# Kernel optimization log

Hardware: AMD Instinct MI355X
Metric: run time of the kernel (lower is better)

Reference implementation:

```python
import jax, jax.numpy as jnp
import numpy as np
import math

B, S, D, H, L, F, V, C = 8, 1024, 768, 12, 6, 3072, 32000, 10
DK = D // H
EPS = 1e-5


def _pos_encoding(seq_len, d):
    pos = jnp.arange(seq_len, dtype=jnp.float32)[:, None]
    div = jnp.exp(jnp.arange(0, d, 2, dtype=jnp.float32) * (-math.log(10000.0) / d))
    pe = jnp.zeros((seq_len, d), dtype=jnp.float32)
    pe = pe.at[:, 0::2].set(jnp.sin(pos * div))
    pe = pe.at[:, 1::2].set(jnp.cos(pos * div))
    return pe


def _layernorm(x, scale, bias):
    mu = jnp.mean(x, axis=-1, keepdims=True)
    var = jnp.mean(jnp.square(x - mu), axis=-1, keepdims=True)
    return (x - mu) * jax.lax.rsqrt(var + EPS) * scale + bias


def setup_inputs() -> dict:
    key = jax.random.key(0)
    ks = jax.random.split(key, 14)
    s = 0.02
    return {
        "tokens": jax.random.randint(ks[0], (B, S), 0, V),
        "emb": jax.random.normal(ks[1], (V, D), jnp.float32) * s,
        "Wq": jax.random.normal(ks[2], (L, D, D), jnp.float32) * s,
        "Wk": jax.random.normal(ks[3], (L, D, D), jnp.float32) * s,
        "Wv": jax.random.normal(ks[4], (L, D, D), jnp.float32) * s,
        "Wo": jax.random.normal(ks[5], (L, D, D), jnp.float32) * s,
        "W1": jax.random.normal(ks[6], (L, D, F), jnp.float32) * s,
        "W2": jax.random.normal(ks[7], (L, F, D), jnp.float32) * s,
        "ln1_s": jnp.ones((L, D), jnp.float32),
        "ln1_b": jnp.zeros((L, D), jnp.float32),
        "ln2_s": jnp.ones((L, D), jnp.float32),
        "ln2_b": jnp.zeros((L, D), jnp.float32),
        "Wc": jax.random.normal(ks[8], (D, C), jnp.float32) * s,
        "bc": jnp.zeros((C,), jnp.float32),
    }


def _block(x, p):
    Wq, Wk, Wv, Wo, W1, W2, l1s, l1b, l2s, l2b = p
    b, s = x.shape[0], x.shape[1]
    q = (x @ Wq).reshape(b, s, H, DK)
    k = (x @ Wk).reshape(b, s, H, DK)
    v = (x @ Wv).reshape(b, s, H, DK)
    scores = jnp.einsum("bqhd,bkhd->bhqk", q, k) / math.sqrt(DK)
    attn = jax.nn.softmax(scores, axis=-1)
    out = jnp.einsum("bhqk,bkhd->bqhd", attn, v).reshape(b, s, D) @ Wo
    x = _layernorm(x + out, l1s, l1b)
    ffn = jax.nn.relu(x @ W1) @ W2
    x = _layernorm(x + ffn, l2s, l2b)
    return x


def reference(tokens, emb, Wq, Wk, Wv, Wo, W1, W2, ln1_s, ln1_b, ln2_s, ln2_b, Wc, bc):
    x = emb[tokens] + _pos_encoding(tokens.shape[1], D)[None]

    def step(h, p):
        return _block(h, p), None

    x, _ = jax.lax.scan(step, x, (Wq, Wk, Wv, Wo, W1, W2, ln1_s, ln1_b, ln2_s, ln2_b))
    pooled = jnp.mean(x, axis=1)  # [B, D]
    return pooled @ Wc + bc
```

## Files before the change

### kernel.cpp

```cpp
#include <hip/hip_runtime.h>
#include <hip/hip_bf16.h>
#include <math.h>

#define BB 8
#define SS 1024
#define DD 768
#define HH 12
#define LL 6
#define FF 3072
#define CC 10
#define BS_ (BB * SS)

typedef __attribute__((ext_vector_type(8))) short short8v;
typedef __attribute__((ext_vector_type(4))) float f32x4;
typedef __attribute__((ext_vector_type(16))) float f32x16;
typedef __attribute__((ext_vector_type(8))) unsigned short ushort8v;
typedef __attribute__((ext_vector_type(4))) unsigned short ushort4v;
typedef __attribute__((ext_vector_type(4))) unsigned int uint4v;

__device__ inline unsigned short f2bf(float f) {
  unsigned int u = __builtin_bit_cast(unsigned int, f);
  u += 0x7fffu + ((u >> 16) & 1u);
  return (unsigned short)(u >> 16);
}
__device__ inline float bf2f(unsigned short u) {
  return __builtin_bit_cast(float, (unsigned int)u << 16);
}
__device__ inline unsigned int cvtpk(float lo, float hi) {
  unsigned int r;
  asm("v_cvt_pk_bf16_f32 %0, %1, %2" : "=v"(r) : "v"(lo), "v"(hi));
  return r;
}
__device__ inline void plswap(unsigned int& a, unsigned int& b) {
  asm volatile("v_permlane32_swap_b32 %0, %1" : "+v"(a), "+v"(b));
}
__device__ inline void gload16(const void* g, void* l) {
  __builtin_amdgcn_global_load_lds((const __attribute__((address_space(1))) void*)g,
                                   (__attribute__((address_space(3))) void*)l, 16, 0, 0);
}

__device__ inline float wave_sum(float v) {
#pragma unroll
  for (int off = 32; off > 0; off >>= 1) v += __shfl_down(v, off);
  return v;
}

__global__ __launch_bounds__(256) void k_embed(const int* __restrict__ tokens,
                                               const float* __restrict__ emb,
                                               ushort* __restrict__ xb) {
  int row = blockIdx.x;
  int s = row & (SS - 1);
  int tok = tokens[row];
  const float* e = emb + (size_t)tok * DD;
  ushort* xbr = xb + (size_t)row * DD;
  for (int d = threadIdx.x; d < DD; d += 256) {
    float freq = expf((float)(d & ~1) * -0.0119926306f);
    float ang = (float)s * freq;
    float pe = (d & 1) ? cosf(ang) : sinf(ang);
    xbr[d] = f2bf(e[d] + pe);
  }
}

__global__ __launch_bounds__(256) void k_transpose_all(
    const float* __restrict__ wq, const float* __restrict__ wk,
    const float* __restrict__ wv, const float* __restrict__ wo,
    const float* __restrict__ w1, const float* __restrict__ w2,
    ushort* __restrict__ wqkv_t, ushort* __restrict__ wo_t,
    ushort* __restrict__ w1_t, ushort* __restrict__ w2_t) {
  __shared__ float tile[32][33];
  int bid = blockIdx.x;
  const float* W; ushort* Wt; int K, N, lb;
  if (bid < 1728) {
    int m = bid / 576; lb = bid - m * 576;
    W = (m == 0) ? wq : (m == 1) ? wk : wv;
    Wt = wqkv_t + m * 768 * 768; K = 768; N = 768;
  } else if (bid < 2304) {
    W = wo; Wt = wo_t; K = 768; N = 768; lb = bid - 1728;
  } else if (bid < 4608) {
    W = w1; Wt = w1_t; K = 768; N = 3072; lb = bid - 2304;
  } else {
    W = w2; Wt = w2_t; K = 3072; N = 768; lb = bid - 4608;
  }
  int nbk = K >> 5;
  int k0 = (lb % nbk) * 32, n0 = (lb / nbk) * 32;
  int t = threadIdx.x;
  int r = t >> 3, c4 = (t & 7) * 4;
  float4 v = *(const float4*)(W + (size_t)(k0 + r) * N + n0 + c4);
  tile[r][c4 + 0] = v.x; tile[r][c4 + 1] = v.y;
  tile[r][c4 + 2] = v.z; tile[r][c4 + 3] = v.w;
  __syncthreads();
  ushort4v o;
#pragma unroll
  for (int i = 0; i < 4; ++i) o[i] = f2bf(tile[c4 + i][r]);
  *(ushort4v*)(Wt + (size_t)(n0 + r) * K + k0 + c4) = o;
}

template <int RELU, int TN>
__global__ __launch_bounds__(256) void k_gemm_db(const ushort* __restrict__ A,
                                                 const ushort* __restrict__ Bt,
                                                 ushort* __restrict__ Cout,
                                                 int M, int N, int K) {
  constexpr int NF = TN / 32;
  __shared__ ushort smem[2][(128 + TN) * 64];
  int bidl = blockIdx.y * gridDim.x + blockIdx.x;
  int nwg = gridDim.x * gridDim.y;
  int cpx = nwg >> 3;
  int tid = (bidl & 7) * cpx + (bidl >> 3);
  int n0 = (tid % gridDim.x) * TN, m0 = (tid / gridDim.x) * 128;
  int t = threadIdx.x, w = t >> 6, l = t & 63;
  int wr = (w >> 1) * 64, wc = (w & 1) * (TN / 2);
  int lr = l & 15, lg = l >> 4;
  f32x4 acc[4][NF] = {};
  int sr8 = l >> 3;
  int scw = ((l & 7) ^ sr8) * 8;
  const ushort* ag = A + (size_t)(m0 + w * 8 + sr8) * K + scw;
  const ushort* bg = Bt + (size_t)(n0 + w * 8 + sr8) * K + scw;
  int nk = K >> 6;
  {
    ushort* al = &smem[0][(w * 8) * 64];
    ushort* bl = &smem[0][128 * 64 + (w * 8) * 64];
#pragma unroll
    for (int ii = 0; ii < 4; ++ii) gload16(ag + (size_t)ii * 32 * K, al + ii * 2048);
#pragma unroll
    for (int ii = 0; ii < TN / 32; ++ii) gload16(bg + (size_t)ii * 32 * K, bl + ii * 2048);
  }
  int rsw = lr & 7;
  for (int k = 0; k < nk; ++k) {
    __syncthreads();
    if (k + 1 < nk) {
      int kb = (k + 1) & 1;
      int kc0 = (k + 1) * 64;
      ushort* al = &smem[kb][(w * 8) * 64];
      ushort* bl = &smem[kb][128 * 64 + (w * 8) * 64];
#pragma unroll
      for (int ii = 0; ii < 4; ++ii) gload16(ag + (size_t)ii * 32 * K + kc0, al + ii * 2048);
#pragma unroll
      for (int ii = 0; ii < TN / 32; ++ii) gload16(bg + (size_t)ii * 32 * K + kc0, bl + ii * 2048);
    }
    const ushort* As = &smem[k & 1][0];
    const ushort* Bs = &smem[k & 1][128 * 64];
#pragma unroll
    for (int ks = 0; ks < 2; ++ks) {
      short8v af[4], bfr[NF];
#pragma unroll
      for (int mi = 0; mi < 4; ++mi)
        af[mi] = *(const short8v*)(As + (wr + mi * 16 + lr) * 64 + (((ks * 4 + lg) ^ rsw) << 3));
#pragma unroll
      for (int ni = 0; ni < NF; ++ni)
        bfr[ni] = *(const short8v*)(Bs + (wc + ni * 16 + lr) * 64 + (((ks * 4 + lg) ^ rsw) << 3));
      __builtin_amdgcn_s_setprio(1);
#pragma unroll
      for (int mi = 0; mi < 4; ++mi)
#pragma unroll
        for (int ni = 0; ni < NF; ++ni)
          acc[mi][ni] = __builtin_amdgcn_mfma_f32_16x16x32_bf16(af[mi], bfr[ni], acc[mi][ni], 0, 0, 0);
      __builtin_amdgcn_s_setprio(0);
    }
  }
  __syncthreads();
  ushort* cst = &smem[0][0];
#pragma unroll
  for (int mi = 0; mi < 4; ++mi)
#pragma unroll
    for (int ni = 0; ni < NF; ++ni) {
      int cl = wc + ni * 16 + lr;
#pragma unroll
      for (int i = 0; i < 4; ++i) {
        int rl = wr + mi * 16 + lg * 4 + i;
        float v = acc[mi][ni][i];
        if (RELU) v = fmaxf(v, 0.f);
        cst[rl * TN + (cl ^ (((rl >> 2) & 3) << 4))] = f2bf(v);
      }
    }
  __syncthreads();
  {
    int row = t >> 1, half = t & 1;
    int swr = ((row >> 2) & 3) << 4;
    ushort* crow = Cout + (size_t)(m0 + row) * N + n0 + half * (TN / 2);
#pragma unroll
    for (int c8 = 0; c8 < TN / 16; ++c8) {
      int c = half * (TN / 2) + c8 * 8;
      ushort8v vv = *(const ushort8v*)(&cst[row * TN + (c ^ swr)]);
      *(ushort8v*)(crow + c8 * 8) = vv;
    }
  }
}

__global__ __launch_bounds__(256) void k_flash(const ushort* __restrict__ qkv,
                                               ushort* __restrict__ ao) {
  __shared__ ushort Ks[2][64][64];
  __shared__ ushort Vt[2][64][64];
  const int LD = 2304;
  int bidl = blockIdx.y * gridDim.x + blockIdx.x;
  int tid = (bidl & 7) * 96 + (bidl >> 3);
  int qt = tid & 7;
  int bh = tid >> 3;
  int hd = bh % HH, b = bh / HH;
  int t = threadIdx.x, w = t >> 6, l = t & 63;
  int q = l & 31, hl = l >> 5;
  int q0 = qt * 128;
  const ushort* qbase = qkv + (size_t)(b * SS) * LD + hd * 64;
  const ushort* kbase = qbase + 768;
  const ushort* vbase = qbase + 1536;
  short8v qfb[4];
  {
    const ushort* qrow = qbase + (size_t)(q0 + w * 32 + q) * LD + hl * 8;
    qfb[0] = *(const short8v*)(qrow);
    qfb[1] = *(const short8v*)(qrow + 16);
    qfb[2] = *(const short8v*)(qrow + 32);
    qfb[3] = *(const short8v*)(qrow + 48);
  }
  const float CEXP = 0.125f * 1.44269504f;
  float l_run = 0.f;
  f32x16 o_acc[2] = {};
  int r8_ = l >> 3;
  const ushort* kgA = kbase + (size_t)(w * 16 + r8_) * LD +
                      (((l & 7) ^ r8_ ^ ((2 * w) & 3)) * 8);
  const ushort* kgB = kbase + (size_t)(w * 16 + 8 + r8_) * LD +
                      (((l & 7) ^ r8_ ^ ((2 * w + 1) & 3)) * 8);
  int d_ = t & 7;
  int dk0 = d_ * 8;
  int kv2 = (t >> 3) * 2;
  const ushort* vg = vbase + (size_t)kv2 * LD + dk0;
  {
    gload16(kgA, &Ks[0][w * 16][0]);
    gload16(kgB, &Ks[0][w * 16 + 8][0]);
    ushort8v v0 = *(const ushort8v*)(vg);
    ushort8v v1 = *(const ushort8v*)(vg + LD);
#pragma unroll
    for (int i = 0; i < 8; ++i) {
      unsigned int pk = (unsigned int)v0[i] | ((unsigned int)v1[i] << 16);
      *(unsigned int*)(&Vt[0][dk0 + i][kv2 ^ (((i ^ d_) & 7) << 3)]) = pk;
    }
  }
  for (int kt = 0; kt < 16; ++kt) {
    int cur = kt & 1, nxt = cur ^ 1;
    __syncthreads();
    ushort8v v0n, v1n;
    if (kt < 15) {
      size_t off = (size_t)(kt + 1) * 64 * LD;
      gload16(kgA + off, &Ks[nxt][w * 16][0]);
      gload16(kgB + off, &Ks[nxt][w * 16 + 8][0]);
      const ushort* vgn = vg + off;
      v0n = *(const ushort8v*)(vgn);
      v1n = *(const ushort8v*)(vgn + LD);
    }
    f32x16 s[2] = {};
    __builtin_amdgcn_s_setprio(1);
#pragma unroll
    for (int c = 0; c < 4; ++c)
#pragma unroll
      for (int mi = 0; mi < 2; ++mi) {
        int gr = ((c << 1) | hl) ^ (l & 7) ^ ((l >> 3) & 3);
        short8v kf = *(const short8v*)(&Ks[cur][mi * 32 + q][gr << 3]);
        s[mi] = __builtin_amdgcn_mfma_f32_32x32x16_bf16(kf, qfb[c], s[mi], 0, 0, 0);
      }
    __builtin_amdgcn_s_setprio(0);
    float psum = 0.f;
#pragma unroll
    for (int mi = 0; mi < 2; ++mi)
#pragma unroll
      for (int r = 0; r < 16; ++r) {
        float e = exp2f(s[mi][r] * CEXP);
        s[mi][r] = e;
        psum += e;
      }
    psum += __shfl_xor(psum, 32);
    l_run += psum;
    short8v pfb[4];
#pragma unroll
    for (int mi = 0; mi < 2; ++mi)
#pragma unroll
      for (int k2 = 0; k2 < 2; ++k2) {
        unsigned int a0 = cvtpk(s[mi][8 * k2 + 0], s[mi][8 * k2 + 1]);
        unsigned int a1 = cvtpk(s[mi][8 * k2 + 2], s[mi][8 * k2 + 3]);
        unsigned int b0 = cvtpk(s[mi][8 * k2 + 4], s[mi][8 * k2 + 5]);
        unsigned int b1 = cvtpk(s[mi][8 * k2 + 6], s[mi][8 * k2 + 7]);
        plswap(a0, b0);
        plswap(a1, b1);
        uint4v u;
        u[0] = a0; u[1] = a1; u[2] = b0; u[3] = b1;
        pfb[mi * 2 + k2] = __builtin_bit_cast(short8v, u);
      }
    if (kt < 15) {
#pragma unroll
      for (int i = 0; i < 8; ++i) {
        unsigned int pk = (unsigned int)v0n[i] | ((unsigned int)v1n[i] << 16);
        *(unsigned int*)(&Vt[nxt][dk0 + i][kv2 ^ (((i ^ d_) & 7) << 3)]) = pk;
      }
    }
    __builtin_amdgcn_s_setprio(1);
#pragma unroll
    for (int ks = 0; ks < 4; ++ks)
#pragma unroll
      for (int od = 0; od < 2; ++od) {
        int vsw = ((l & 7) ^ ((od * 4) | ((l >> 3) & 3))) & 7;
        short8v vf = *(const short8v*)(
            &Vt[cur][od * 32 + q][(((ks << 1) | hl) ^ vsw) << 3]);
        o_acc[od] = __builtin_amdgcn_mfma_f32_32x32x16_bf16(vf, pfb[ks], o_acc[od], 0, 0, 0);
      }
    __builtin_amdgcn_s_setprio(0);
  }
  __syncthreads();
  float invl = 1.f / l_run;
  ushort* otile = &Ks[0][0][0] + w * 2048;
#pragma unroll
  for (int od = 0; od < 2; ++od)
#pragma unroll
    for (int r = 0; r < 16; r += 2) {
      unsigned int pk = cvtpk(o_acc[od][r] * invl, o_acc[od][r + 1] * invl);
      int c = od * 32 + 8 * (r >> 2) + 4 * hl + (r & 3);
      *(unsigned int*)(&otile[q * 64 + (c ^ ((q & 7) << 3))]) = pk;
    }
  __syncthreads();
  {
    int r2 = l >> 1, hf = l & 1;
    ushort* orow = ao + (size_t)(b * SS + q0 + w * 32 + r2) * DD + hd * 64 + hf * 32;
#pragma unroll
    for (int k = 0; k < 4; ++k) {
      int c = hf * 32 + k * 8;
      ushort8v vv = *(const ushort8v*)(&otile[r2 * 64 + (c ^ ((r2 & 7) << 3))]);
      *(ushort8v*)(orow + k * 8) = vv;
    }
  }
}

__global__ __launch_bounds__(64) void k_addln(ushort* __restrict__ xb,
                                              const ushort* __restrict__ y,
                                              const float* __restrict__ sc,
                                              const float* __restrict__ bi) {
  int row = blockIdx.x, l = threadIdx.x;
  int d0 = l * 12;
  ushort* xr = xb + (size_t)row * DD;
  const ushort* yr = y + (size_t)row * DD;
  ushort4v xa[3], ya[3];
#pragma unroll
  for (int j = 0; j < 3; ++j) {
    xa[j] = *(const ushort4v*)(xr + d0 + j * 4);
    ya[j] = *(const ushort4v*)(yr + d0 + j * 4);
  }
  float v[12];
  float s = 0.f;
#pragma unroll
  for (int j = 0; j < 3; ++j)
#pragma unroll
    for (int i = 0; i < 4; ++i) {
      float vv = bf2f(xa[j][i]) + bf2f(ya[j][i]);
      v[j * 4 + i] = vv;
      s += vv;
    }
  float mu = wave_sum(s);
  mu = __shfl(mu, 0) * (1.f / 768.f);
  float vs = 0.f;
#pragma unroll
  for (int i = 0; i < 12; ++i) {
    float c = v[i] - mu;
    vs += c * c;
  }
  vs = wave_sum(vs);
  float rstd = rsqrtf(__shfl(vs, 0) * (1.f / 768.f) + 1e-5f);
  float4 scv[3], biv[3];
#pragma unroll
  for (int j = 0; j < 3; ++j) {
    scv[j] = *(const float4*)(sc + d0 + j * 4);
    biv[j] = *(const float4*)(bi + d0 + j * 4);
  }
#pragma unroll
  for (int j = 0; j < 3; ++j) {
    ushort4v o;
    const float* sj = (const float*)&scv[j];
    const float* bj = (const float*)&biv[j];
#pragma unroll
    for (int i = 0; i < 4; ++i) o[i] = f2bf((v[j * 4 + i] - mu) * rstd * sj[i] + bj[i]);
    *(ushort4v*)(xr + d0 + j * 4) = o;
  }
}

__global__ __launch_bounds__(256) void k_pool(const ushort* __restrict__ xb,
                                              float* __restrict__ pooled) {
  int b = blockIdx.x, chunk = blockIdx.y, t = threadIdx.x;
  float a0 = 0, a1 = 0, a2 = 0;
  for (int s2 = chunk * 128; s2 < chunk * 128 + 128; ++s2) {
    const ushort* xr = xb + (size_t)(b * SS + s2) * DD;
    a0 += bf2f(xr[t]); a1 += bf2f(xr[t + 256]); a2 += bf2f(xr[t + 512]);
  }
  atomicAdd(&pooled[b * DD + t], a0 * (1.f / 1024.f));
  atomicAdd(&pooled[b * DD + t + 256], a1 * (1.f / 1024.f));
  atomicAdd(&pooled[b * DD + t + 512], a2 * (1.f / 1024.f));
}

__global__ __launch_bounds__(64) void k_cls(const float* __restrict__ pooled,
                                            const float* __restrict__ Wc,
                                            const float* __restrict__ bc,
                                            float* __restrict__ out) {
  int idx = blockIdx.x;
  int b = idx / CC, c = idx % CC;
  int t = threadIdx.x;
  float acc = 0.f;
  for (int d0 = t; d0 < DD; d0 += 64) acc = fmaf(pooled[b * DD + d0], Wc[d0 * CC + c], acc);
  acc = wave_sum(acc);
  if (t == 0) out[b * CC + c] = acc + bc[c];
}

extern "C" void kernel_launch(void* const* d_in, const int* in_sizes, int n_in,
                              void* d_out, int out_size, void* d_ws, size_t ws_size,
                              hipStream_t stream) {
  (void)in_sizes; (void)n_in; (void)out_size; (void)ws_size;
  const int* tokens = (const int*)d_in[0];
  const float* emb = (const float*)d_in[1];
  const float* Wq = (const float*)d_in[2];
  const float* Wk = (const float*)d_in[3];
  const float* Wv = (const float*)d_in[4];
  const float* Wo = (const float*)d_in[5];
  const float* W1 = (const float*)d_in[6];
  const float* W2 = (const float*)d_in[7];
  const float* l1s = (const float*)d_in[8];
  const float* l1b = (const float*)d_in[9];
  const float* l2s = (const float*)d_in[10];
  const float* l2b = (const float*)d_in[11];
  const float* Wc = (const float*)d_in[12];
  const float* bc = (const float*)d_in[13];
  float* out = (float*)d_out;

  char* p = (char*)d_ws;
  ushort* xb = (ushort*)p;              p += (size_t)BS_ * DD * 2;
  ushort* qkvb = (ushort*)p;
  ushort* hb = (ushort*)p;
  ushort* ao = (ushort*)(p + (size_t)BS_ * 2304 * 2);
  p += (size_t)BS_ * FF * 2;
  ushort* yb = (ushort*)p;              p += (size_t)BS_ * DD * 2;
  ushort* wt = (ushort*)p;              p += (size_t)(2304 * 768 + 768 * 768 + 3072 * 768 + 768 * 3072) * 2;
  float* pooled = (float*)p;

  ushort* wqkv_t = wt;
  ushort* wo_t = wqkv_t + 2304 * 768;
  ushort* w1_t = wo_t + 768 * 768;
  ushort* w2_t = w1_t + 3072 * 768;

  k_embed<<<BS_, 256, 0, stream>>>(tokens, emb, xb);

  for (int l = 0; l < LL; ++l) {
    k_transpose_all<<<6912, 256, 0, stream>>>(
        Wq + (size_t)l * DD * DD, Wk + (size_t)l * DD * DD,
        Wv + (size_t)l * DD * DD, Wo + (size_t)l * DD * DD,
        W1 + (size_t)l * DD * FF, W2 + (size_t)l * FF * DD,
        wqkv_t, wo_t, w1_t, w2_t);

    k_gemm_db<0, 128><<<dim3(2304 / 128, BS_ / 128), 256, 0, stream>>>(xb, wqkv_t, qkvb, BS_, 2304, DD);
    k_flash<<<dim3(SS / 128, BB * HH), 256, 0, stream>>>(qkvb, ao);
    k_gemm_db<0, 64><<<dim3(DD / 64, BS_ / 128), 256, 0, stream>>>(ao, wo_t, yb, BS_, DD, DD);
    k_addln<<<BS_, 64, 0, stream>>>(xb, yb, l1s + l * DD, l1b + l * DD);
    k_gemm_db<1, 128><<<dim3(FF / 128, BS_ / 128), 256, 0, stream>>>(xb, w1_t, hb, BS_, FF, DD);
    k_gemm_db<0, 64><<<dim3(DD / 64, BS_ / 128), 256, 0, stream>>>(hb, w2_t, yb, BS_, DD, FF);
    k_addln<<<BS_, 64, 0, stream>>>(xb, yb, l2s + l * DD, l2b + l * DD);
  }

  hipMemsetAsync(pooled, 0, (size_t)BB * DD * sizeof(float), stream);
  k_pool<<<dim3(BB, 8), 256, 0, stream>>>(xb, pooled);
  k_cls<<<BB * CC, 64, 0, stream>>>(pooled, Wc, bc, out);
}
```

Baseline: 1.448 ms.

## Widen flash-attention blocks to 256 queries and fold softmax scale into QKV GEMM

The attention kernel now runs 512 threads (8 waves) per block and covers 256 query rows. Each K/V tile staged in LDS is therefore shared by twice as many waves, which halves global K/V traffic and the number of blocks. The softmax scale and log2(e) factor are multiplied into the Q columns in the QKV GEMM epilogue, which removes a per-score multiply in the attention loop. In exchange, larger blocks may reduce occupancy or tail balance. Q is also rounded to bf16 after scaling, which slightly changes numerics.

```diff
diff --git a/kernel.cpp b/kernel.cpp
--- a/kernel.cpp
+++ b/kernel.cpp
@@ -17,6 +17,8 @@
 typedef __attribute__((ext_vector_type(8))) unsigned short ushort8v;
 typedef __attribute__((ext_vector_type(4))) unsigned short ushort4v;
 typedef __attribute__((ext_vector_type(4))) unsigned int uint4v;
+
+#define CEXPQ 0.18033688f
 
 __device__ inline unsigned short f2bf(float f) {
   unsigned int u = __builtin_bit_cast(unsigned int, f);
@@ -95,7 +97,7 @@
   *(ushort4v*)(Wt + (size_t)(n0 + r) * K + k0 + c4) = o;
 }
 
-template <int RELU, int TN>
+template <int RELU, int TN, int SCALEQ = 0>
 __global__ __launch_bounds__(256) void k_gemm_db(const ushort* __restrict__ A,
                                                  const ushort* __restrict__ Bt,
                                                  ushort* __restrict__ Cout,
@@ -158,6 +160,7 @@
     }
   }
   __syncthreads();
+  float osc = (SCALEQ && n0 < 768) ? CEXPQ : 1.0f;
   ushort* cst = &smem[0][0];
 #pragma unroll
   for (int mi = 0; mi < 4; ++mi)
@@ -169,6 +172,7 @@
         int rl = wr + mi * 16 + lg * 4 + i;
         float v = acc[mi][ni][i];
         if (RELU) v = fmaxf(v, 0.f);
+        if (SCALEQ) v *= osc;
         cst[rl * TN + (cl ^ (((rl >> 2) & 3) << 4))] = f2bf(v);
       }
     }
@@ -186,19 +190,20 @@
   }
 }
 
-__global__ __launch_bounds__(256) void k_flash(const ushort* __restrict__ qkv,
+__global__ __launch_bounds__(512) void k_flash(const ushort* __restrict__ qkv,
                                                ushort* __restrict__ ao) {
-  __shared__ ushort Ks[2][64][64];
-  __shared__ ushort Vt[2][64][64];
+  __shared__ ushort lds[16384];
+  ushort* KsB = lds;
+  ushort* VtB = lds + 8192;
   const int LD = 2304;
   int bidl = blockIdx.y * gridDim.x + blockIdx.x;
-  int tid = (bidl & 7) * 96 + (bidl >> 3);
-  int qt = tid & 7;
-  int bh = tid >> 3;
+  int tid = (bidl & 7) * 48 + (bidl >> 3);
+  int qt = tid & 3;
+  int bh = tid >> 2;
   int hd = bh % HH, b = bh / HH;
   int t = threadIdx.x, w = t >> 6, l = t & 63;
   int q = l & 31, hl = l >> 5;
-  int q0 = qt * 128;
+  int q0 = qt * 256;
   const ushort* qbase = qkv + (size_t)(b * SS) * LD + hd * 64;
   const ushort* kbase = qbase + 768;
   const ushort* vbase = qbase + 1536;
@@ -210,40 +215,35 @@
     qfb[2] = *(const short8v*)(qrow + 32);
     qfb[3] = *(const short8v*)(qrow + 48);
   }
-  const float CEXP = 0.125f * 1.44269504f;
   float l_run = 0.f;
   f32x16 o_acc[2] = {};
   int r8_ = l >> 3;
-  const ushort* kgA = kbase + (size_t)(w * 16 + r8_) * LD +
-                      (((l & 7) ^ r8_ ^ ((2 * w) & 3)) * 8);
-  const ushort* kgB = kbase + (size_t)(w * 16 + 8 + r8_) * LD +
-                      (((l & 7) ^ r8_ ^ ((2 * w + 1) & 3)) * 8);
-  int d_ = t & 7;
-  int dk0 = d_ * 8;
-  int kv2 = (t >> 3) * 2;
-  const ushort* vg = vbase + (size_t)kv2 * LD + dk0;
+  const ushort* kg = kbase + (size_t)(w * 8 + r8_) * LD +
+                     (((l & 7) ^ r8_ ^ (w & 3)) * 8);
+  int d4 = (t & 15) * 4;
+  int kv2 = (t >> 4) * 2;
+  const ushort* vg = vbase + (size_t)kv2 * LD + d4;
   {
-    gload16(kgA, &Ks[0][w * 16][0]);
-    gload16(kgB, &Ks[0][w * 16 + 8][0]);
-    ushort8v v0 = *(const ushort8v*)(vg);
-    ushort8v v1 = *(const ushort8v*)(vg + LD);
-#pragma unroll
-    for (int i = 0; i < 8; ++i) {
-      unsigned int pk = (unsigned int)v0[i] | ((unsigned int)v1[i] << 16);
-      *(unsigned int*)(&Vt[0][dk0 + i][kv2 ^ (((i ^ d_) & 7) << 3)]) = pk;
+    gload16(kg, KsB + (w * 8) * 64);
+    ushort4v v0 = *(const ushort4v*)(vg);
+    ushort4v v1 = *(const ushort4v*)(vg + LD);
+#pragma unroll
+    for (int i = 0; i < 4; ++i) {
+      int row = d4 + i;
+      int swz = ((row & 7) ^ ((row >> 3) & 7)) & 7;
+      *(unsigned int*)(VtB + row * 64 + (kv2 ^ (swz << 3))) =
+          (unsigned int)v0[i] | ((unsigned int)v1[i] << 16);
     }
   }
   for (int kt = 0; kt < 16; ++kt) {
     int cur = kt & 1, nxt = cur ^ 1;
     __syncthreads();
-    ushort8v v0n, v1n;
+    ushort4v v0n, v1n;
     if (kt < 15) {
       size_t off = (size_t)(kt + 1) * 64 * LD;
-      gload16(kgA + off, &Ks[nxt][w * 16][0]);
-      gload16(kgB + off, &Ks[nxt][w * 16 + 8][0]);
-      const ushort* vgn = vg + off;
-      v0n = *(const ushort8v*)(vgn);
-      v1n = *(const ushort8v*)(vgn + LD);
+      gload16(kg + off, KsB + nxt * 4096 + (w * 8) * 64);
+      v0n = *(const ushort4v*)(vg + off);
+      v1n = *(const ushort4v*)(vg + off + LD);
     }
     f32x16 s[2] = {};
     __builtin_amdgcn_s_setprio(1);
@@ -252,7 +252,7 @@
 #pragma unroll
       for (int mi = 0; mi < 2; ++mi) {
         int gr = ((c << 1) | hl) ^ (l & 7) ^ ((l >> 3) & 3);
-        short8v kf = *(const short8v*)(&Ks[cur][mi * 32 + q][gr << 3]);
+        short8v kf = *(const short8v*)(KsB + cur * 4096 + (mi * 32 + q) * 64 + (gr << 3));
         s[mi] = __builtin_amdgcn_mfma_f32_32x32x16_bf16(kf, qfb[c], s[mi], 0, 0, 0);
       }
     __builtin_amdgcn_s_setprio(0);
@@ -261,7 +261,7 @@
     for (int mi = 0; mi < 2; ++mi)
 #pragma unroll
       for (int r = 0; r < 16; ++r) {
-        float e = exp2f(s[mi][r] * CEXP);
+        float e = exp2f(s[mi][r]);
         s[mi][r] = e;
         psum += e;
       }
@@ -284,9 +284,11 @@
       }
     if (kt < 15) {
 #pragma unroll
-      for (int i = 0; i < 8; ++i) {
-        unsigned int pk = (unsigned int)v0n[i] | ((unsigned int)v1n[i] << 16);
-        *(unsigned int*)(&Vt[nxt][dk0 + i][kv2 ^ (((i ^ d_) & 7) << 3)]) = pk;
+      for (int i = 0; i < 4; ++i) {
+        int row = d4 + i;
+        int swz = ((row & 7) ^ ((row >> 3) & 7)) & 7;
+        *(unsigned int*)(VtB + nxt * 4096 + row * 64 + (kv2 ^ (swz << 3))) =
+            (unsigned int)v0n[i] | ((unsigned int)v1n[i] << 16);
       }
     }
     __builtin_amdgcn_s_setprio(1);
@@ -296,14 +298,14 @@
       for (int od = 0; od < 2; ++od) {
         int vsw = ((l & 7) ^ ((od * 4) | ((l >> 3) & 3))) & 7;
         short8v vf = *(const short8v*)(
-            &Vt[cur][od * 32 + q][(((ks << 1) | hl) ^ vsw) << 3]);
+            VtB + cur * 4096 + (od * 32 + q) * 64 + ((((ks << 1) | hl) ^ vsw) << 3));
         o_acc[od] = __builtin_amdgcn_mfma_f32_32x32x16_bf16(vf, pfb[ks], o_acc[od], 0, 0, 0);
       }
     __builtin_amdgcn_s_setprio(0);
   }
   __syncthreads();
   float invl = 1.f / l_run;
-  ushort* otile = &Ks[0][0][0] + w * 2048;
+  ushort* otile = lds + w * 2048;
 #pragma unroll
   for (int od = 0; od < 2; ++od)
 #pragma unroll
@@ -446,8 +448,8 @@
         W1 + (size_t)l * DD * FF, W2 + (size_t)l * FF * DD,
         wqkv_t, wo_t, w1_t, w2_t);
 
-    k_gemm_db<0, 128><<<dim3(2304 / 128, BS_ / 128), 256, 0, stream>>>(xb, wqkv_t, qkvb, BS_, 2304, DD);
-    k_flash<<<dim3(SS / 128, BB * HH), 256, 0, stream>>>(qkvb, ao);
+    k_gemm_db<0, 128, 1><<<dim3(2304 / 128, BS_ / 128), 256, 0, stream>>>(xb, wqkv_t, qkvb, BS_, 2304, DD);
+    k_flash<<<dim3(SS / 256, BB * HH), 512, 0, stream>>>(qkvb, ao);
     k_gemm_db<0, 64><<<dim3(DD / 64, BS_ / 128), 256, 0, stream>>>(ao, wo_t, yb, BS_, DD, DD);
     k_addln<<<BS_, 64, 0, stream>>>(xb, yb, l1s + l * DD, l1b + l * DD);
     k_gemm_db<1, 128><<<dim3(FF / 128, BS_ / 128), 256, 0, stream>>>(xb, w1_t, hb, BS_, FF, DD);
```

Result: slower. 1.504 ms (+3.9%).
